# Performance work log

Measured on AMD Instinct MI355X. Metric: run time of the kernel, lower is better.

Reference implementation:

```python
import jax, jax.numpy as jnp
import numpy as np
from jax import lax

EPS = 1e-6


def layernorm2d(x, w, b):
    # channel LayerNorm over dim C of NCHW (biased variance), matching LayerNormFunction
    mu = jnp.mean(x, axis=1, keepdims=True)
    var = jnp.mean((x - mu) ** 2, axis=1, keepdims=True)
    y = (x - mu) * lax.rsqrt(var + EPS)
    return w[None, :, None, None] * y + b[None, :, None, None]


def conv1x1(x, W, b):
    # x: (N,C,H,W), W: (O,C), b: (O,)
    return jnp.einsum('nchw,oc->nohw', x, W) + b[None, :, None, None]


def conv3x3(x, W, b):
    # W: (O,I,3,3)
    y = lax.conv_general_dilated(x, W, window_strides=(1, 1), padding='SAME',
                                 dimension_numbers=('NCHW', 'OIHW', 'NCHW'))
    return y + b[None, :, None, None]


def avg_pool3x3(x):
    # torch F.avg_pool2d k=3, s=1, p=1, count_include_pad=True -> always divide by 9
    s = lax.reduce_window(x, 0.0, lax.add, (1, 1, 3, 3), (1, 1, 1, 1),
                          [(0, 0), (0, 0), (1, 1), (1, 1)])
    return s / 9.0


def setup_inputs() -> dict:
    key = jax.random.key(0)
    N, C, H, W = 8, 64, 128, 256
    ks = jax.random.split(key, 12)
    d = {
        'x_l': jax.random.normal(ks[0], (N, C, H, W), jnp.float32),
        'x_r': jax.random.normal(ks[1], (N, C, H, W), jnp.float32),
        'nl_w': jnp.ones((C,), jnp.float32),
        'nl_b': jnp.zeros((C,), jnp.float32),
        'nr_w': jnp.ones((C,), jnp.float32),
        'nr_b': jnp.zeros((C,), jnp.float32),
        'Wq_l': jax.random.normal(ks[2], (C, C), jnp.float32) * 0.05,
        'bq_l': jax.random.normal(ks[3], (C,), jnp.float32) * 0.05,
        'Wq_r': jax.random.normal(ks[4], (C, C), jnp.float32) * 0.05,
        'bq_r': jax.random.normal(ks[5], (C,), jnp.float32) * 0.05,
        'Wv_r': jax.random.normal(ks[6], (C, C), jnp.float32) * 0.05,
        'bv_r': jax.random.normal(ks[7], (C,), jnp.float32) * 0.05,
        'beta': jax.random.normal(ks[8], (1, C, 1, 1), jnp.float32) * 0.1,
        'gamma': jax.random.normal(ks[9], (1, C, 1, 1), jnp.float32) * 0.1,
        'W_hf': jax.random.normal(ks[10], (C, C, 3, 3), jnp.float32) * 0.02,
        'b_hf': jax.random.normal(ks[11], (C,), jnp.float32) * 0.02,
    }
    return d


def reference(x_l, x_r, nl_w, nl_b, nr_w, nr_b, Wq_l, bq_l, Wq_r, bq_r,
              Wv_r, bv_r, beta, gamma, W_hf, b_hf):
    C = x_l.shape[1]
    scale = C ** (-0.5)

    # Projections (1x1 convs); Q_l, Q_r, V_r as (N,H,W,C)
    Q_l = jnp.transpose(conv1x1(layernorm2d(x_l, nl_w, nl_b), Wq_l, bq_l), (0, 2, 3, 1))
    Q_r = jnp.transpose(conv1x1(layernorm2d(x_r, nr_w, nr_b), Wq_r, bq_r), (0, 2, 3, 1))
    V_r = jnp.transpose(conv1x1(x_r, Wv_r, bv_r), (0, 2, 3, 1))

    # Per-scanline cross attention: (N,H,W,W)
    attn = jnp.einsum('nhwc,nhvc->nhwv', Q_l, Q_r) * scale
    attn = jax.nn.softmax(attn, axis=-1)
    F_r2l = jnp.einsum('nhwv,nhvc->nhwc', attn, V_r)  # (N,H,W,C)
    F_r2l = jnp.transpose(F_r2l, (0, 3, 1, 2)) * beta  # (N,C,H,W)

    # High-frequency branch
    hf = conv3x3(x_r - avg_pool3x3(x_r), W_hf, b_hf)

    return x_l + F_r2l + gamma * hf
```

## Files before the change

### kernel.cpp

```cpp
#include <hip/hip_runtime.h>
#include <hip/hip_bf16.h>

#define N_ 8
#define C_ 64
#define H_ 128
#define W_ 256
#define HW_ (H_*W_)
#define CHW_ (C_*H_*W_)

typedef unsigned int u32;
typedef unsigned short u16;
typedef float f32x4 __attribute__((ext_vector_type(4)));
typedef short bf16x8 __attribute__((ext_vector_type(8)));

__device__ __forceinline__ float blo(u32 u) { return __uint_as_float(u << 16); }
__device__ __forceinline__ float bhi(u32 u) { return __uint_as_float(u & 0xffff0000u); }
__device__ __forceinline__ u16 f2bf(float f) {
    u32 u = __float_as_uint(f);
    u32 lsb = (u >> 16) & 1u;
    u += 0x7fffu + lsb;
    return (u16)(u >> 16);
}
__device__ __forceinline__ u32 pack2(float a, float b) {
    return (u32)f2bf(a) | ((u32)f2bf(b) << 16);
}
__device__ __forceinline__ int rmap(int px) {
    return (px & 0xF8) | ((px + (px >> 3)) & 7);
}

__global__ __launch_bounds__(512) void k_fused(
    const float* __restrict__ xl, const float* __restrict__ xr,
    const float* __restrict__ nlw, const float* __restrict__ nlb,
    const float* __restrict__ nrw, const float* __restrict__ nrb,
    const float* __restrict__ Wql, const float* __restrict__ bql,
    const float* __restrict__ Wqr, const float* __restrict__ bqr,
    const float* __restrict__ Wvr, const float* __restrict__ bvr,
    const float* __restrict__ beta, float* __restrict__ out)
{
    __shared__ u32 B1[8192];
    __shared__ u32 B2[8192];
    __shared__ uint4 Ks[2048];
    __shared__ float muA[256], rsA[256];
    __shared__ float SlA[64], BlA[64], SrA[64], BrA[64], BvA[64];
    const int tid  = threadIdx.x;
    const int lane = tid & 63, wv = tid >> 6;
    const int l15  = lane & 15, kg = lane >> 4;
    const int mw   = wv & 3;
    const int nh   = wv >> 2;
    const int blk  = blockIdx.x;
    const int n = blk >> 7, h = blk & 127;
    const size_t gbase = (size_t)n*CHW_ + (size_t)h*W_;

    if (tid < 64) {
        const int o = tid;
        float sl = 0.f, bl = bql[o], sr = 0.f, br = bqr[o];
        for (int c = 0; c < 64; ++c) {
            float wl = Wql[o*64+c], wr = Wqr[o*64+c];
            sl += wl * nlw[c];
            bl += wl * nlb[c];
            sr += wr * nrw[c];
            br += wr * nrb[c];
        }
        SlA[o] = sl; BlA[o] = bl; SrA[o] = sr; BrA[o] = br; BvA[o] = bvr[o];
    }

    const int oA = mw*16 + l15;
    bf16x8 aL[2], aR[2], aV[2];
    #pragma unroll
    for (int hf = 0; hf < 2; ++hf) {
        bf16x8 tl, tr, tv;
        #pragma unroll
        for (int j = 0; j < 8; ++j) {
            const int c = hf*32 + kg*8 + j;
            tl[j] = (short)f2bf(Wql[oA*64+c] * nlw[c]);
            tr[j] = (short)f2bf(Wqr[oA*64+c] * nrw[c]);
            tv[j] = (short)f2bf(Wvr[oA*64+c]);
        }
        aL[hf] = tl; aR[hf] = tr; aV[hf] = tv;
    }

    {
        const int chunk = tid >> 6;
        const int j = tid & 63;
        const int c0 = chunk*8;
        float4 v[8];
        #pragma unroll
        for (int e = 0; e < 8; ++e)
            v[e] = *(const float4*)(xl + gbase + (size_t)(c0+e)*HW_ + j*4);
        #pragma unroll
        for (int t = 0; t < 4; ++t) {
            const int px = j*4 + t;
            const int r = rmap(px);
            u32 q0,q1,q2,q3;
            const float* f0 = (const float*)&v[0]; const float* f1 = (const float*)&v[1];
            const float* f2 = (const float*)&v[2]; const float* f3 = (const float*)&v[3];
            const float* f4 = (const float*)&v[4]; const float* f5 = (const float*)&v[5];
            const float* f6 = (const float*)&v[6]; const float* f7 = (const float*)&v[7];
            asm("v_cvt_pk_bf16_f32 %0, %1, %2" : "=v"(q0) : "v"(f0[t]), "v"(f1[t]));
            asm("v_cvt_pk_bf16_f32 %0, %1, %2" : "=v"(q1) : "v"(f2[t]), "v"(f3[t]));
            asm("v_cvt_pk_bf16_f32 %0, %1, %2" : "=v"(q2) : "v"(f4[t]), "v"(f5[t]));
            asm("v_cvt_pk_bf16_f32 %0, %1, %2" : "=v"(q3) : "v"(f6[t]), "v"(f7[t]));
            uint4 pv; pv.x=q0; pv.y=q1; pv.z=q2; pv.w=q3;
            *(uint4*)&B1[r*32 + ((chunk ^ (r&7))<<2)] = pv;
        }
    }
    __syncthreads();
    if (tid < 256) {
        const int px = tid;
        const int r = rmap(px);
        float sum = 0.f, ssq = 0.f;
        #pragma unroll
        for (int c8 = 0; c8 < 8; ++c8) {
            uint4 val = *(const uint4*)&B1[r*32 + ((c8 ^ (r&7))<<2)];
            const u32* wp = (const u32*)&val;
            #pragma unroll
            for (int q = 0; q < 4; ++q) {
                float a = blo(wp[q]), b = bhi(wp[q]);
                sum += a + b; ssq += a*a + b*b;
            }
        }
        float mu = sum * (1.f/64.f);
        float var = ssq * (1.f/64.f) - mu*mu;
        muA[px] = mu;
        rsA[px] = rsqrtf(var + 1e-6f);
    }
    __syncthreads();
    {
        float Sv[4], Bv[4];
        #pragma unroll
        for (int r4 = 0; r4 < 4; ++r4) {
            Sv[r4] = SlA[mw*16 + kg*4 + r4];
            Bv[r4] = BlA[mw*16 + kg*4 + r4];
        }
        #pragma unroll
        for (int nt2 = 0; nt2 < 8; ++nt2) {
            const int nt = nh*8 + nt2;
            const int px = nt*16 + l15;
            const int r = rmap(px);
            f32x4 d = {0.f,0.f,0.f,0.f};
            #pragma unroll
            for (int hf = 0; hf < 2; ++hf) {
                bf16x8 b = *(const bf16x8*)&B1[r*32 + (((hf*4+kg) ^ (r&7))<<2)];
                d = __builtin_amdgcn_mfma_f32_16x16x32_bf16(aL[hf], b, d, 0, 0, 0);
            }
            const float mu = muA[px], rs = rsA[px];
            uint2 pv;
            pv.x = pack2(rs*(d[0] - mu*Sv[0]) + Bv[0], rs*(d[1] - mu*Sv[1]) + Bv[1]);
            pv.y = pack2(rs*(d[2] - mu*Sv[2]) + Bv[2], rs*(d[3] - mu*Sv[3]) + Bv[3]);
            const int ci = (mw*2 + (kg>>1)) ^ (px & 7);
            *(uint2*)&B2[px*32 + (ci<<2) + (kg&1)*2] = pv;
        }
    }
    __syncthreads();

    bf16x8 qf[2][2];
    #pragma unroll
    for (int ntq = 0; ntq < 2; ++ntq)
        #pragma unroll
        for (int ci = 0; ci < 2; ++ci) {
            const int q = wv*32 + ntq*16 + l15;
            qf[ntq][ci] = *(const bf16x8*)&B2[q*32 + (((ci*4+kg) ^ (q&7))<<2)];
        }
    {
        const int chunk = tid >> 6;
        const int j = tid & 63;
        const int c0 = chunk*8;
        float4 v[8];
        #pragma unroll
        for (int e = 0; e < 8; ++e)
            v[e] = *(const float4*)(xr + gbase + (size_t)(c0+e)*HW_ + j*4);
        #pragma unroll
        for (int t = 0; t < 4; ++t) {
            const int px = j*4 + t;
            const int r = rmap(px);
            u32 q0,q1,q2,q3;
            const float* f0 = (const float*)&v[0]; const float* f1 = (const float*)&v[1];
            const float* f2 = (const float*)&v[2]; const float* f3 = (const float*)&v[3];
            const float* f4 = (const float*)&v[4]; const float* f5 = (const float*)&v[5];
            const float* f6 = (const float*)&v[6]; const float* f7 = (const float*)&v[7];
            asm("v_cvt_pk_bf16_f32 %0, %1, %2" : "=v"(q0) : "v"(f0[t]), "v"(f1[t]));
            asm("v_cvt_pk_bf16_f32 %0, %1, %2" : "=v"(q1) : "v"(f2[t]), "v"(f3[t]));
            asm("v_cvt_pk_bf16_f32 %0, %1, %2" : "=v"(q2) : "v"(f4[t]), "v"(f5[t]));
            asm("v_cvt_pk_bf16_f32 %0, %1, %2" : "=v"(q3) : "v"(f6[t]), "v"(f7[t]));
            uint4 pv; pv.x=q0; pv.y=q1; pv.z=q2; pv.w=q3;
            *(uint4*)&B1[r*32 + ((chunk ^ (r&7))<<2)] = pv;
        }
    }
    __syncthreads();
    if (tid < 256) {
        const int px = tid;
        const int r = rmap(px);
        float sum = 0.f, ssq = 0.f;
        #pragma unroll
        for (int c8 = 0; c8 < 8; ++c8) {
            uint4 val = *(const uint4*)&B1[r*32 + ((c8 ^ (r&7))<<2)];
            const u32* wp = (const u32*)&val;
            #pragma unroll
            for (int q = 0; q < 4; ++q) {
                float a = blo(wp[q]), b = bhi(wp[q]);
                sum += a + b; ssq += a*a + b*b;
            }
        }
        float mu = sum * (1.f/64.f);
        float var = ssq * (1.f/64.f) - mu*mu;
        muA[px] = mu;
        rsA[px] = rsqrtf(var + 1e-6f);
    }
    __syncthreads();
    {
        float Sv[4], Bv[4];
        #pragma unroll
        for (int r4 = 0; r4 < 4; ++r4) {
            Sv[r4] = SrA[mw*16 + kg*4 + r4];
            Bv[r4] = BrA[mw*16 + kg*4 + r4];
        }
        const int chv = mw*16 + l15;
        const float vbias = BvA[chv];
        u32* KsW = (u32*)Ks;
        u16* Vts = (u16*)B2;
        #pragma unroll
        for (int nt2 = 0; nt2 < 8; ++nt2) {
            const int nt = nh*8 + nt2;
            const int px = nt*16 + l15;
            const int r = rmap(px);
            bf16x8 bX[2];
            #pragma unroll
            for (int hf = 0; hf < 2; ++hf)
                bX[hf] = *(const bf16x8*)&B1[r*32 + (((hf*4+kg) ^ (r&7))<<2)];
            f32x4 dq = {0.f,0.f,0.f,0.f};
            f32x4 dv = {0.f,0.f,0.f,0.f};
            #pragma unroll
            for (int hf = 0; hf < 2; ++hf) {
                dq = __builtin_amdgcn_mfma_f32_16x16x32_bf16(aR[hf], bX[hf], dq, 0, 0, 0);
                dv = __builtin_amdgcn_mfma_f32_16x16x32_bf16(bX[hf], aV[hf], dv, 0, 0, 0);
            }
            const float mu = muA[px], rs = rsA[px];
            uint2 pq;
            pq.x = pack2(rs*(dq[0] - mu*Sv[0]) + Bv[0], rs*(dq[1] - mu*Sv[1]) + Bv[1]);
            pq.y = pack2(rs*(dq[2] - mu*Sv[2]) + Bv[2], rs*(dq[3] - mu*Sv[3]) + Bv[3]);
            const int ciq = (mw*2 + (kg>>1)) ^ (px & 7);
            *(uint2*)&KsW[px*32 + (ciq<<2) + (kg&1)*2] = pq;
            uint2 pw;
            pw.x = pack2(dv[0] + vbias, dv[1] + vbias);
            pw.y = pack2(dv[2] + vbias, dv[3] + vbias);
            const int swz = (nt*2 + (kg>>1)) ^ (chv & 7);
            *(uint2*)&Vts[chv*256 + (swz<<3) + (kg&1)*4] = pw;
        }
    }
    __syncthreads();

    f32x4 oacc[2][4];
    #pragma unroll
    for (int a = 0; a < 2; ++a)
        #pragma unroll
        for (int b = 0; b < 4; ++b)
            oacc[a][b] = (f32x4){0.f,0.f,0.f,0.f};
    float lsum[2] = {0.f,0.f};
    u32* Pw = &B1[wv*512];
    const u16* Vts = (const u16*)B2;

    for (int kb = 0; kb < 8; ++kb) {
        f32x4 st[2][2];
        #pragma unroll
        for (int mt = 0; mt < 2; ++mt)
            #pragma unroll
            for (int nt = 0; nt < 2; ++nt)
                st[mt][nt] = (f32x4){0.f,0.f,0.f,0.f};
        #pragma unroll
        for (int ci = 0; ci < 2; ++ci) {
            bf16x8 a0 = *(const bf16x8*)&Ks[(kb*32 +      l15)*8 + ((ci*4 + kg) ^ (l15 & 7))];
            bf16x8 a1 = *(const bf16x8*)&Ks[(kb*32 + 16 + l15)*8 + ((ci*4 + kg) ^ (l15 & 7))];
            #pragma unroll
            for (int nt = 0; nt < 2; ++nt) {
                st[0][nt] = __builtin_amdgcn_mfma_f32_16x16x32_bf16(a0, qf[nt][ci], st[0][nt], 0, 0, 0);
                st[1][nt] = __builtin_amdgcn_mfma_f32_16x16x32_bf16(a1, qf[nt][ci], st[1][nt], 0, 0, 0);
            }
        }
        #pragma unroll
        for (int nt = 0; nt < 2; ++nt) {
            const int ql = nt*16 + l15;
            #pragma unroll
            for (int mt = 0; mt < 2; ++mt) {
                float p0 = __expf(st[mt][nt][0]*0.125f);
                float p1 = __expf(st[mt][nt][1]*0.125f);
                float p2 = __expf(st[mt][nt][2]*0.125f);
                float p3 = __expf(st[mt][nt][3]*0.125f);
                lsum[nt] += (p0+p1)+(p2+p3);
                u32 pr0, pr1;
                asm("v_cvt_pk_bf16_f32 %0, %1, %2" : "=v"(pr0) : "v"(p0), "v"(p1));
                asm("v_cvt_pk_bf16_f32 %0, %1, %2" : "=v"(pr1) : "v"(p2), "v"(p3));
                const int c16 = (2*mt + (kg >> 1)) ^ (ql & 3);
                uint2 pv; pv.x = pr0; pv.y = pr1;
                *(uint2*)&Pw[ql*16 + c16*4 + (kg & 1)*2] = pv;
            }
        }
        asm volatile("s_waitcnt lgkmcnt(0)" ::: "memory");
        bf16x8 vb[4];
        #pragma unroll
        for (int nc = 0; nc < 4; ++nc)
            vb[nc] = *(const bf16x8*)&Vts[(nc*16 + l15)*256 + ((kb*4 + kg) ^ (l15 & 7))*8];
        #pragma unroll
        for (int qt = 0; qt < 2; ++qt) {
            const int ql = qt*16 + l15;
            bf16x8 pa = *(const bf16x8*)&Pw[ql*16 + (kg ^ (ql & 3))*4];
            #pragma unroll
            for (int nc = 0; nc < 4; ++nc)
                oacc[qt][nc] = __builtin_amdgcn_mfma_f32_16x16x32_bf16(pa, vb[nc], oacc[qt][nc], 0, 0, 0);
        }
    }

    #pragma unroll
    for (int nt = 0; nt < 2; ++nt) {
        float s = lsum[nt];
        s += __shfl_xor(s, 16, 64);
        s += __shfl_xor(s, 32, 64);
        lsum[nt] = s;
    }
    float linv[2][4];
    #pragma unroll
    for (int qt = 0; qt < 2; ++qt)
        #pragma unroll
        for (int r = 0; r < 4; ++r)
            linv[qt][r] = 1.0f / __shfl(lsum[qt], kg*4 + r, 64);

    float* PwF = (float*)Pw;
    const size_t obase = gbase + wv*32;
    #pragma unroll
    for (int nc = 0; nc < 4; ++nc) {
        asm volatile("s_waitcnt lgkmcnt(0)" ::: "memory");
        #pragma unroll
        for (int qt = 0; qt < 2; ++qt) {
            f32x4 vals;
            vals[0] = oacc[qt][nc][0]*linv[qt][0];
            vals[1] = oacc[qt][nc][1]*linv[qt][1];
            vals[2] = oacc[qt][nc][2]*linv[qt][2];
            vals[3] = oacc[qt][nc][3]*linv[qt][3];
            *(f32x4*)&PwF[l15*32 + (((qt*4 + kg) ^ (l15 & 7))<<2)] = vals;
        }
        asm volatile("s_waitcnt lgkmcnt(0)" ::: "memory");
        #pragma unroll
        for (int it = 0; it < 8; ++it) {
            const int csub = it*2 + (lane >> 5);
            const int qloc = lane & 31;
            float v = PwF[csub*32 + ((((qloc >> 2)) ^ (csub & 7))<<2) + (qloc & 3)];
            const int ch = nc*16 + csub;
            size_t gidx = obase + (size_t)ch*HW_ + qloc;
            out[gidx] = xl[gidx] + beta[ch]*v + out[gidx];
        }
    }
}

__global__ __launch_bounds__(256) void k_hipass(
    const float* __restrict__ xr, u16* __restrict__ Tt)
{
    __shared__ u16 Ts[64*256];
    const int bid = blockIdx.x;
    const int blk = (bid & 7)*128 + (bid >> 3);
    const int n = blk >> 7, h = blk & 127;
    const int tid = threadIdx.x;
    const int lane = tid & 63, wv = tid >> 6;
    const float* rowp = xr + (size_t)n*CHW_ + (size_t)h*W_ + lane*4;

    #pragma unroll
    for (int ci = 0; ci < 16; ++ci) {
        const int c = wv*16 + ci;
        const float* pc = rowp + (size_t)c*HW_;
        float ctr0=0.f, ctr1=0.f, ctr2=0.f, ctr3=0.f;
        float s0=0.f, s1=0.f, s2=0.f, s3=0.f;
        #pragma unroll
        for (int dy = -1; dy <= 1; ++dy) {
            const int hh = h + dy;
            float4 v = {0.f,0.f,0.f,0.f};
            if (hh >= 0 && hh < 128) v = *(const float4*)(pc + dy*W_);
            float lft = __shfl_up(v.w, 1);
            float rgt = __shfl_down(v.x, 1);
            if (lane == 0)  lft = 0.f;
            if (lane == 63) rgt = 0.f;
            s0 += lft + v.x + v.y;
            s1 += v.x + v.y + v.z;
            s2 += v.y + v.z + v.w;
            s3 += v.z + v.w + rgt;
            if (dy == 0) { ctr0=v.x; ctr1=v.y; ctr2=v.z; ctr3=v.w; }
        }
        uint2 pv;
        pv.x = pack2(ctr0 - s0*(1.f/9.f), ctr1 - s1*(1.f/9.f));
        pv.y = pack2(ctr2 - s2*(1.f/9.f), ctr3 - s3*(1.f/9.f));
        const int swz = (c >> 3) << 3;
        *(uint2*)&Ts[c*256 + ((lane*4) ^ swz)] = pv;
    }
    __syncthreads();
    uint4* gout = (uint4*)(Tt + (size_t)blk*256*64);
    #pragma unroll
    for (int iter = 0; iter < 8; ++iter) {
        const int lin = iter*256 + tid;
        const int px = lin >> 3, chunk = lin & 7;
        const int pxs = px ^ (chunk << 3);
        u32 w4[4];
        #pragma unroll
        for (int tp = 0; tp < 4; ++tp) {
            const int c0 = chunk*8 + tp*2;
            u16 a = Ts[(c0    )*256 + pxs];
            u16 b = Ts[(c0 + 1)*256 + pxs];
            w4[tp] = (u32)a | ((u32)b << 16);
        }
        uint4 v; v.x=w4[0]; v.y=w4[1]; v.z=w4[2]; v.w=w4[3];
        gout[lin] = v;
    }
}

__device__ __forceinline__ void conv_tile(
    const uint4* __restrict__ buf, const bf16x8* A,
    const float* gv, const float* bv,
    int n, int h, int w0, int mt, int l15, int kg,
    float* __restrict__ out)
{
    f32x4 acc[4] = {{0,0,0,0},{0,0,0,0},{0,0,0,0},{0,0,0,0}};
    #pragma unroll
    for (int s = 0; s < 18; ++s) {
        const int q  = s >> 1;
        const int dy = q / 3, dx = q % 3;
        const int c0 = (s & 1)*4 + kg;
        #pragma unroll
        for (int nt = 0; nt < 4; ++nt) {
            const int wt = nt*16 + l15 + dx;
            bf16x8 b = *(const bf16x8*)&buf[(dy*66 + wt)*8 + (c0 ^ (wt & 7))];
            acc[nt] = __builtin_amdgcn_mfma_f32_16x16x32_bf16(A[s], b, acc[nt], 0, 0, 0);
        }
    }
    #pragma unroll
    for (int nt = 0; nt < 4; ++nt) {
        const int px = w0 + nt*16 + l15;
        #pragma unroll
        for (int r = 0; r < 4; ++r) {
            const int oo = mt*16 + kg*4 + r;
            size_t idx = (size_t)(n*64 + oo)*HW_ + (size_t)h*W_ + px;
            out[idx] = gv[r]*(acc[nt][r] + bv[r]);
        }
    }
}

__global__ __launch_bounds__(256) void k_conv(
    const u16* __restrict__ Tt, const float* __restrict__ Whf,
    const float* __restrict__ bhf, const float* __restrict__ gam,
    float* __restrict__ out)
{
    __shared__ uint4 Xs[2][1584];
    const int tid  = threadIdx.x;
    const int lane = tid & 63;
    const int mt   = tid >> 6;
    const int l15  = lane & 15;
    const int kg   = lane >> 4;
    const int bid  = blockIdx.x;
    const int blk2 = (bid & 7)*256 + (bid >> 3);
    const int row  = blk2 >> 1, half = blk2 & 1;
    const int n = row >> 7, h = row & 127;
    const int w00 = half*128;
    const int w01 = w00 + 64;

    const int oa = mt*16 + l15;
    bf16x8 A[18];
    #pragma unroll
    for (int s = 0; s < 18; ++s) {
        const int q  = s >> 1;
        const int ib = (s & 1)*32 + kg*8;
        bf16x8 a;
        #pragma unroll
        for (int j = 0; j < 8; ++j) {
            float wv = Whf[(size_t)(oa*64 + ib + j)*9 + q];
            a[j] = (short)f2bf(wv);
        }
        A[s] = a;
    }
    float gv[4], bv[4];
    #pragma unroll
    for (int r = 0; r < 4; ++r) {
        int oo = mt*16 + kg*4 + r;
        gv[r] = gam[oo];
        bv[r] = bhf[oo];
    }

    for (int it = tid; it < 1584; it += 256) {
        int dy    = it / 528;
        int rem   = it - dy*528;
        int wt    = rem >> 3;
        int chunk = rem & 7;
        int hh = h + dy - 1;
        int wg = w00 + wt - 1;
        uint4 v = {0,0,0,0};
        if (hh >= 0 && hh < 128 && wg >= 0 && wg < 256)
            v = *(const uint4*)(Tt + (((size_t)(n*128 + hh)*256 + wg)*64 + chunk*8));
        Xs[0][(dy*66 + wt)*8 + (chunk ^ (wt & 7))] = v;
    }
    __syncthreads();

    uint4 rr[7];
    #pragma unroll
    for (int k = 0; k < 7; ++k) {
        const int it = k*256 + tid;
        if (it < 1584) {
            int dy    = it / 528;
            int rem   = it - dy*528;
            int wt    = rem >> 3;
            int chunk = rem & 7;
            int hh = h + dy - 1;
            int wg = w01 + wt - 1;
            uint4 v = {0,0,0,0};
            if (hh >= 0 && hh < 128 && wg >= 0 && wg < 256)
                v = *(const uint4*)(Tt + (((size_t)(n*128 + hh)*256 + wg)*64 + chunk*8));
            rr[k] = v;
        }
    }

    conv_tile(&Xs[0][0], A, gv, bv, n, h, w00, mt, l15, kg, out);

    #pragma unroll
    for (int k = 0; k < 7; ++k) {
        const int it = k*256 + tid;
        if (it < 1584) {
            int dy    = it / 528;
            int rem   = it - dy*528;
            int wt    = rem >> 3;
            int chunk = rem & 7;
            Xs[1][(dy*66 + wt)*8 + (chunk ^ (wt & 7))] = rr[k];
        }
    }
    __syncthreads();
    conv_tile(&Xs[1][0], A, gv, bv, n, h, w01, mt, l15, kg, out);
}

extern "C" void kernel_launch(void* const* d_in, const int* in_sizes, int n_in,
                              void* d_out, int out_size, void* d_ws, size_t ws_size,
                              hipStream_t stream)
{
    const float* xl   = (const float*)d_in[0];
    const float* xr   = (const float*)d_in[1];
    const float* nlw  = (const float*)d_in[2];
    const float* nlb  = (const float*)d_in[3];
    const float* nrw  = (const float*)d_in[4];
    const float* nrb  = (const float*)d_in[5];
    const float* Wql  = (const float*)d_in[6];
    const float* bql  = (const float*)d_in[7];
    const float* Wqr  = (const float*)d_in[8];
    const float* bqr  = (const float*)d_in[9];
    const float* Wvr  = (const float*)d_in[10];
    const float* bvr  = (const float*)d_in[11];
    const float* beta = (const float*)d_in[12];
    const float* gam  = (const float*)d_in[13];
    const float* Whf  = (const float*)d_in[14];
    const float* bhf  = (const float*)d_in[15];
    float* out = (float*)d_out;

    u16* Tt = (u16*)d_ws;

    k_hipass<<<1024, 256, 0, stream>>>(xr, Tt);
    k_conv<<<2048, 256, 0, stream>>>(Tt, Whf, bhf, gam, out);
    k_fused<<<1024, 512, 0, stream>>>(xl, xr, nlw, nlb, nrw, nrb,
                                      Wql, bql, Wqr, bqr, Wvr, bvr,
                                      beta, out);
}
```

Before: 176.5 us.

## Split block into left/right wave halves processing both projections concurrently

The block's 8 waves are split into two halves: waves 0-3 load x_l, compute its layernorm stats and the Q_l projection, while waves 4-7 do the same for x_r plus K and V. Previously these ran one after another with all waves. This removes several barriers and serial phases, so the global loads for both images overlap. In exchange, each wave now holds 16 tiles of packed Q/V results in registers before writing them to shared memory, which raises register pressure.

Measured after the change: 200.4 us. 1.14x slower.

```diff
diff --git a/kernel.cpp b/kernel.cpp
--- a/kernel.cpp
+++ b/kernel.cpp
@@ -39,14 +39,15 @@
 {
     __shared__ u32 B1[8192];
     __shared__ u32 B2[8192];
-    __shared__ uint4 Ks[2048];
-    __shared__ float muA[256], rsA[256];
+    __shared__ u32 B3[8192];
+    __shared__ float muL[256], rsL[256], muR[256], rsR[256];
     __shared__ float SlA[64], BlA[64], SrA[64], BrA[64], BvA[64];
     const int tid  = threadIdx.x;
     const int lane = tid & 63, wv = tid >> 6;
     const int l15  = lane & 15, kg = lane >> 4;
+    const int side = wv >> 2;
     const int mw   = wv & 3;
-    const int nh   = wv >> 2;
+    const int htid = tid & 255;
     const int blk  = blockIdx.x;
     const int n = blk >> 7, h = blk & 127;
     const size_t gbase = (size_t)n*CHW_ + (size_t)h*W_;
@@ -66,52 +67,73 @@
 
     const int oA = mw*16 + l15;
     bf16x8 aL[2], aR[2], aV[2];
-    #pragma unroll
-    for (int hf = 0; hf < 2; ++hf) {
-        bf16x8 tl, tr, tv;
-        #pragma unroll
-        for (int j = 0; j < 8; ++j) {
-            const int c = hf*32 + kg*8 + j;
-            tl[j] = (short)f2bf(Wql[oA*64+c] * nlw[c]);
-            tr[j] = (short)f2bf(Wqr[oA*64+c] * nrw[c]);
-            tv[j] = (short)f2bf(Wvr[oA*64+c]);
-        }
-        aL[hf] = tl; aR[hf] = tr; aV[hf] = tv;
+    if (side == 0) {
+        #pragma unroll
+        for (int hf = 0; hf < 2; ++hf) {
+            bf16x8 tl;
+            #pragma unroll
+            for (int j = 0; j < 8; ++j) {
+                const int c = hf*32 + kg*8 + j;
+                tl[j] = (short)f2bf(Wql[oA*64+c] * nlw[c]);
+            }
+            aL[hf] = tl;
+        }
+    } else {
+        #pragma unroll
+        for (int hf = 0; hf < 2; ++hf) {
+            bf16x8 tr, tv;
+            #pragma unroll
+            for (int j = 0; j < 8; ++j) {
+                const int c = hf*32 + kg*8 + j;
+                tr[j] = (short)f2bf(Wqr[oA*64+c] * nrw[c]);
+                tv[j] = (short)f2bf(Wvr[oA*64+c]);
+            }
+            aR[hf] = tr; aV[hf] = tv;
+        }
     }
 
     {
-        const int chunk = tid >> 6;
-        const int j = tid & 63;
-        const int c0 = chunk*8;
-        float4 v[8];
-        #pragma unroll
-        for (int e = 0; e < 8; ++e)
-            v[e] = *(const float4*)(xl + gbase + (size_t)(c0+e)*HW_ + j*4);
-        #pragma unroll
-        for (int t = 0; t < 4; ++t) {
-            const int px = j*4 + t;
-            const int r = rmap(px);
-            u32 q0,q1,q2,q3;
-            const float* f0 = (const float*)&v[0]; const float* f1 = (const float*)&v[1];
-            const float* f2 = (const float*)&v[2]; const float* f3 = (const float*)&v[3];
-            const float* f4 = (const float*)&v[4]; const float* f5 = (const float*)&v[5];
-            const float* f6 = (const float*)&v[6]; const float* f7 = (const float*)&v[7];
-            asm("v_cvt_pk_bf16_f32 %0, %1, %2" : "=v"(q0) : "v"(f0[t]), "v"(f1[t]));
-            asm("v_cvt_pk_bf16_f32 %0, %1, %2" : "=v"(q1) : "v"(f2[t]), "v"(f3[t]));
-            asm("v_cvt_pk_bf16_f32 %0, %1, %2" : "=v"(q2) : "v"(f4[t]), "v"(f5[t]));
-            asm("v_cvt_pk_bf16_f32 %0, %1, %2" : "=v"(q3) : "v"(f6[t]), "v"(f7[t]));
-            uint4 pv; pv.x=q0; pv.y=q1; pv.z=q2; pv.w=q3;
-            *(uint4*)&B1[r*32 + ((chunk ^ (r&7))<<2)] = pv;
-        }
-    }
-    __syncthreads();
-    if (tid < 256) {
-        const int px = tid;
+        const float* xsrc = side ? xr : xl;
+        u32* XB = side ? B2 : B1;
+        #pragma unroll
+        for (int it2 = 0; it2 < 2; ++it2) {
+            const int g = it2*256 + htid;
+            const int chunk = g >> 6;
+            const int j = g & 63;
+            const int c0 = chunk*8;
+            float4 v[8];
+            #pragma unroll
+            for (int e = 0; e < 8; ++e)
+                v[e] = *(const float4*)(xsrc + gbase + (size_t)(c0+e)*HW_ + j*4);
+            #pragma unroll
+            for (int t = 0; t < 4; ++t) {
+                const int px = j*4 + t;
+                const int r = rmap(px);
+                u32 q0,q1,q2,q3;
+                const float* f0 = (const float*)&v[0]; const float* f1 = (const float*)&v[1];
+                const float* f2 = (const float*)&v[2]; const float* f3 = (const float*)&v[3];
+                const float* f4 = (const float*)&v[4]; const float* f5 = (const float*)&v[5];
+                const float* f6 = (const float*)&v[6]; const float* f7 = (const float*)&v[7];
+                asm("v_cvt_pk_bf16_f32 %0, %1, %2" : "=v"(q0) : "v"(f0[t]), "v"(f1[t]));
+                asm("v_cvt_pk_bf16_f32 %0, %1, %2" : "=v"(q1) : "v"(f2[t]), "v"(f3[t]));
+                asm("v_cvt_pk_bf16_f32 %0, %1, %2" : "=v"(q2) : "v"(f4[t]), "v"(f5[t]));
+                asm("v_cvt_pk_bf16_f32 %0, %1, %2" : "=v"(q3) : "v"(f6[t]), "v"(f7[t]));
+                uint4 pv; pv.x=q0; pv.y=q1; pv.z=q2; pv.w=q3;
+                *(uint4*)&XB[r*32 + ((chunk ^ (r&7))<<2)] = pv;
+            }
+        }
+    }
+    __syncthreads();
+    {
+        const u32* XB = side ? B2 : B1;
+        float* muX = side ? muR : muL;
+        float* rsX = side ? rsR : rsL;
+        const int px = htid;
         const int r = rmap(px);
         float sum = 0.f, ssq = 0.f;
         #pragma unroll
         for (int c8 = 0; c8 < 8; ++c8) {
-            uint4 val = *(const uint4*)&B1[r*32 + ((c8 ^ (r&7))<<2)];
+            uint4 val = *(const uint4*)&XB[r*32 + ((c8 ^ (r&7))<<2)];
             const u32* wp = (const u32*)&val;
             #pragma unroll
             for (int q = 0; q < 4; ++q) {
@@ -121,11 +143,13 @@
         }
         float mu = sum * (1.f/64.f);
         float var = ssq * (1.f/64.f) - mu*mu;
-        muA[px] = mu;
-        rsA[px] = rsqrtf(var + 1e-6f);
-    }
-    __syncthreads();
-    {
+        muX[px] = mu;
+        rsX[px] = rsqrtf(var + 1e-6f);
+    }
+    __syncthreads();
+
+    u32 hq[16][2], hv[16][2];
+    if (side == 0) {
         float Sv[4], Bv[4];
         #pragma unroll
         for (int r4 = 0; r4 < 4; ++r4) {
@@ -133,8 +157,7 @@
             Bv[r4] = BlA[mw*16 + kg*4 + r4];
         }
         #pragma unroll
-        for (int nt2 = 0; nt2 < 8; ++nt2) {
-            const int nt = nh*8 + nt2;
+        for (int nt = 0; nt < 16; ++nt) {
             const int px = nt*16 + l15;
             const int r = rmap(px);
             f32x4 d = {0.f,0.f,0.f,0.f};
@@ -143,71 +166,14 @@
                 bf16x8 b = *(const bf16x8*)&B1[r*32 + (((hf*4+kg) ^ (r&7))<<2)];
                 d = __builtin_amdgcn_mfma_f32_16x16x32_bf16(aL[hf], b, d, 0, 0, 0);
             }
-            const float mu = muA[px], rs = rsA[px];
+            const float mu = muL[px], rs = rsL[px];
             uint2 pv;
             pv.x = pack2(rs*(d[0] - mu*Sv[0]) + Bv[0], rs*(d[1] - mu*Sv[1]) + Bv[1]);
             pv.y = pack2(rs*(d[2] - mu*Sv[2]) + Bv[2], rs*(d[3] - mu*Sv[3]) + Bv[3]);
             const int ci = (mw*2 + (kg>>1)) ^ (px & 7);
-            *(uint2*)&B2[px*32 + (ci<<2) + (kg&1)*2] = pv;
-        }
-    }
-    __syncthreads();
-
-    bf16x8 qf[2][2];
-    #pragma unroll
-    for (int ntq = 0; ntq < 2; ++ntq)
-        #pragma unroll
-        for (int ci = 0; ci < 2; ++ci) {
-            const int q = wv*32 + ntq*16 + l15;
-            qf[ntq][ci] = *(const bf16x8*)&B2[q*32 + (((ci*4+kg) ^ (q&7))<<2)];
-        }
-    {
-        const int chunk = tid >> 6;
-        const int j = tid & 63;
-        const int c0 = chunk*8;
-        float4 v[8];
-        #pragma unroll
-        for (int e = 0; e < 8; ++e)
-            v[e] = *(const float4*)(xr + gbase + (size_t)(c0+e)*HW_ + j*4);
-        #pragma unroll
-        for (int t = 0; t < 4; ++t) {
-            const int px = j*4 + t;
-            const int r = rmap(px);
-            u32 q0,q1,q2,q3;
-            const float* f0 = (const float*)&v[0]; const float* f1 = (const float*)&v[1];
-            const float* f2 = (const float*)&v[2]; const float* f3 = (const float*)&v[3];
-            const float* f4 = (const float*)&v[4]; const float* f5 = (const float*)&v[5];
-            const float* f6 = (const float*)&v[6]; const float* f7 = (const float*)&v[7];
-            asm("v_cvt_pk_bf16_f32 %0, %1, %2" : "=v"(q0) : "v"(f0[t]), "v"(f1[t]));
-            asm("v_cvt_pk_bf16_f32 %0, %1, %2" : "=v"(q1) : "v"(f2[t]), "v"(f3[t]));
-            asm("v_cvt_pk_bf16_f32 %0, %1, %2" : "=v"(q2) : "v"(f4[t]), "v"(f5[t]));
-            asm("v_cvt_pk_bf16_f32 %0, %1, %2" : "=v"(q3) : "v"(f6[t]), "v"(f7[t]));
-            uint4 pv; pv.x=q0; pv.y=q1; pv.z=q2; pv.w=q3;
-            *(uint4*)&B1[r*32 + ((chunk ^ (r&7))<<2)] = pv;
-        }
-    }
-    __syncthreads();
-    if (tid < 256) {
-        const int px = tid;
-        const int r = rmap(px);
-        float sum = 0.f, ssq = 0.f;
-        #pragma unroll
-        for (int c8 = 0; c8 < 8; ++c8) {
-            uint4 val = *(const uint4*)&B1[r*32 + ((c8 ^ (r&7))<<2)];
-            const u32* wp = (const u32*)&val;
-            #pragma unroll
-            for (int q = 0; q < 4; ++q) {
-                float a = blo(wp[q]), b = bhi(wp[q]);
-                sum += a + b; ssq += a*a + b*b;
-            }
-        }
-        float mu = sum * (1.f/64.f);
-        float var = ssq * (1.f/64.f) - mu*mu;
-        muA[px] = mu;
-        rsA[px] = rsqrtf(var + 1e-6f);
-    }
-    __syncthreads();
-    {
+            *(uint2*)&B3[px*32 + (ci<<2) + (kg&1)*2] = pv;
+        }
+    } else {
         float Sv[4], Bv[4];
         #pragma unroll
         for (int r4 = 0; r4 < 4; ++r4) {
@@ -216,17 +182,14 @@
         }
         const int chv = mw*16 + l15;
         const float vbias = BvA[chv];
-        u32* KsW = (u32*)Ks;
-        u16* Vts = (u16*)B2;
-        #pragma unroll
-        for (int nt2 = 0; nt2 < 8; ++nt2) {
-            const int nt = nh*8 + nt2;
+        #pragma unroll
+        for (int nt = 0; nt < 16; ++nt) {
             const int px = nt*16 + l15;
             const int r = rmap(px);
             bf16x8 bX[2];
             #pragma unroll
             for (int hf = 0; hf < 2; ++hf)
-                bX[hf] = *(const bf16x8*)&B1[r*32 + (((hf*4+kg) ^ (r&7))<<2)];
+                bX[hf] = *(const bf16x8*)&B2[r*32 + (((hf*4+kg) ^ (r&7))<<2)];
             f32x4 dq = {0.f,0.f,0.f,0.f};
             f32x4 dv = {0.f,0.f,0.f,0.f};
             #pragma unroll
@@ -234,19 +197,38 @@
                 dq = __builtin_amdgcn_mfma_f32_16x16x32_bf16(aR[hf], bX[hf], dq, 0, 0, 0);
                 dv = __builtin_amdgcn_mfma_f32_16x16x32_bf16(bX[hf], aV[hf], dv, 0, 0, 0);
             }
-            const float mu = muA[px], rs = rsA[px];
-            uint2 pq;
-            pq.x = pack2(rs*(dq[0] - mu*Sv[0]) + Bv[0], rs*(dq[1] - mu*Sv[1]) + Bv[1]);
-            pq.y = pack2(rs*(dq[2] - mu*Sv[2]) + Bv[2], rs*(dq[3] - mu*Sv[3]) + Bv[3]);
+            const float mu = muR[px], rs = rsR[px];
+            hq[nt][0] = pack2(rs*(dq[0] - mu*Sv[0]) + Bv[0], rs*(dq[1] - mu*Sv[1]) + Bv[1]);
+            hq[nt][1] = pack2(rs*(dq[2] - mu*Sv[2]) + Bv[2], rs*(dq[3] - mu*Sv[3]) + Bv[3]);
+            hv[nt][0] = pack2(dv[0] + vbias, dv[1] + vbias);
+            hv[nt][1] = pack2(dv[2] + vbias, dv[3] + vbias);
+        }
+    }
+    __syncthreads();
+
+    if (side == 1) {
+        u32* KsW = B2;
+        u16* Vts16 = (u16*)B1;
+        const int chv = mw*16 + l15;
+        #pragma unroll
+        for (int nt = 0; nt < 16; ++nt) {
+            const int px = nt*16 + l15;
             const int ciq = (mw*2 + (kg>>1)) ^ (px & 7);
+            uint2 pq; pq.x = hq[nt][0]; pq.y = hq[nt][1];
             *(uint2*)&KsW[px*32 + (ciq<<2) + (kg&1)*2] = pq;
-            uint2 pw;
-            pw.x = pack2(dv[0] + vbias, dv[1] + vbias);
-            pw.y = pack2(dv[2] + vbias, dv[3] + vbias);
+            uint2 pw; pw.x = hv[nt][0]; pw.y = hv[nt][1];
             const int swz = (nt*2 + (kg>>1)) ^ (chv & 7);
-            *(uint2*)&Vts[chv*256 + (swz<<3) + (kg&1)*4] = pw;
-        }
-    }
+            *(uint2*)&Vts16[chv*256 + (swz<<3) + (kg&1)*4] = pw;
+        }
+    }
+    bf16x8 qf[2][2];
+    #pragma unroll
+    for (int ntq = 0; ntq < 2; ++ntq)
+        #pragma unroll
+        for (int ci = 0; ci < 2; ++ci) {
+            const int q = wv*32 + ntq*16 + l15;
+            qf[ntq][ci] = *(const bf16x8*)&B3[q*32 + (((ci*4+kg) ^ (q&7))<<2)];
+        }
     __syncthreads();
 
     f32x4 oacc[2][4];
@@ -256,8 +238,9 @@
         for (int b = 0; b < 4; ++b)
             oacc[a][b] = (f32x4){0.f,0.f,0.f,0.f};
     float lsum[2] = {0.f,0.f};
-    u32* Pw = &B1[wv*512];
-    const u16* Vts = (const u16*)B2;
+    u32* Pw = &B3[wv*512];
+    const u16* Vts = (const u16*)B1;
+    const uint4* KsR = (const uint4*)B2;
 
     for (int kb = 0; kb < 8; ++kb) {
         f32x4 st[2][2];
@@ -268,8 +251,8 @@
                 st[mt][nt] = (f32x4){0.f,0.f,0.f,0.f};
         #pragma unroll
         for (int ci = 0; ci < 2; ++ci) {
-            bf16x8 a0 = *(const bf16x8*)&Ks[(kb*32 +      l15)*8 + ((ci*4 + kg) ^ (l15 & 7))];
-            bf16x8 a1 = *(const bf16x8*)&Ks[(kb*32 + 16 + l15)*8 + ((ci*4 + kg) ^ (l15 & 7))];
+            bf16x8 a0 = *(const bf16x8*)&KsR[(kb*32 +      l15)*8 + ((ci*4 + kg) ^ (l15 & 7))];
+            bf16x8 a1 = *(const bf16x8*)&KsR[(kb*32 + 16 + l15)*8 + ((ci*4 + kg) ^ (l15 & 7))];
             #pragma unroll
             for (int nt = 0; nt < 2; ++nt) {
                 st[0][nt] = __builtin_amdgcn_mfma_f32_16x16x32_bf16(a0, qf[nt][ci], st[0][nt], 0, 0, 0);
```

## Drop K LDS buffer, pass P via shuffles, store output directly from registers

Applied to the files above, without the earlier changes.

Removes the separate 32KB Ks shared buffer by holding the projected Q/V values in registers, then writing K into B1 after a barrier. This cuts LDS per block, and the launch bound is raised to request 4 blocks per SM. The softmax probability tile is now redistributed into the MFMA A-operand layout with cross-lane shuffles instead of an LDS round trip. The epilogue writes float4 vectors straight from the accumulators, skipping the LDS transpose. The trade-off is higher register pressure under the tighter launch bound, plus an extra barrier.

After: 191.9 us. +8.7%, slower.

```diff
diff --git a/kernel.cpp b/kernel.cpp
--- a/kernel.cpp
+++ b/kernel.cpp
@@ -28,7 +28,7 @@
     return (px & 0xF8) | ((px + (px >> 3)) & 7);
 }
 
-__global__ __launch_bounds__(512) void k_fused(
+__global__ __launch_bounds__(512, 4) void k_fused(
     const float* __restrict__ xl, const float* __restrict__ xr,
     const float* __restrict__ nlw, const float* __restrict__ nlb,
     const float* __restrict__ nrw, const float* __restrict__ nrb,
@@ -39,7 +39,6 @@
 {
     __shared__ u32 B1[8192];
     __shared__ u32 B2[8192];
-    __shared__ uint4 Ks[2048];
     __shared__ float muA[256], rsA[256];
     __shared__ float SlA[64], BlA[64], SrA[64], BrA[64], BvA[64];
     const int tid  = threadIdx.x;
@@ -207,6 +206,8 @@
         rsA[px] = rsqrtf(var + 1e-6f);
     }
     __syncthreads();
+
+    u32 hq[8][2], hv[8][2];
     {
         float Sv[4], Bv[4];
         #pragma unroll
@@ -216,8 +217,6 @@
         }
         const int chv = mw*16 + l15;
         const float vbias = BvA[chv];
-        u32* KsW = (u32*)Ks;
-        u16* Vts = (u16*)B2;
         #pragma unroll
         for (int nt2 = 0; nt2 < 8; ++nt2) {
             const int nt = nh*8 + nt2;
@@ -235,16 +234,26 @@
                 dv = __builtin_amdgcn_mfma_f32_16x16x32_bf16(bX[hf], aV[hf], dv, 0, 0, 0);
             }
             const float mu = muA[px], rs = rsA[px];
-            uint2 pq;
-            pq.x = pack2(rs*(dq[0] - mu*Sv[0]) + Bv[0], rs*(dq[1] - mu*Sv[1]) + Bv[1]);
-            pq.y = pack2(rs*(dq[2] - mu*Sv[2]) + Bv[2], rs*(dq[3] - mu*Sv[3]) + Bv[3]);
+            hq[nt2][0] = pack2(rs*(dq[0] - mu*Sv[0]) + Bv[0], rs*(dq[1] - mu*Sv[1]) + Bv[1]);
+            hq[nt2][1] = pack2(rs*(dq[2] - mu*Sv[2]) + Bv[2], rs*(dq[3] - mu*Sv[3]) + Bv[3]);
+            hv[nt2][0] = pack2(dv[0] + vbias, dv[1] + vbias);
+            hv[nt2][1] = pack2(dv[2] + vbias, dv[3] + vbias);
+        }
+    }
+    __syncthreads();
+    {
+        const int chv = mw*16 + l15;
+        u16* Vts16 = (u16*)B2;
+        #pragma unroll
+        for (int nt2 = 0; nt2 < 8; ++nt2) {
+            const int nt = nh*8 + nt2;
+            const int px = nt*16 + l15;
             const int ciq = (mw*2 + (kg>>1)) ^ (px & 7);
-            *(uint2*)&KsW[px*32 + (ciq<<2) + (kg&1)*2] = pq;
-            uint2 pw;
-            pw.x = pack2(dv[0] + vbias, dv[1] + vbias);
-            pw.y = pack2(dv[2] + vbias, dv[3] + vbias);
+            uint2 pq; pq.x = hq[nt2][0]; pq.y = hq[nt2][1];
+            *(uint2*)&B1[px*32 + (ciq<<2) + (kg&1)*2] = pq;
+            uint2 pw; pw.x = hv[nt2][0]; pw.y = hv[nt2][1];
             const int swz = (nt*2 + (kg>>1)) ^ (chv & 7);
-            *(uint2*)&Vts[chv*256 + (swz<<3) + (kg&1)*4] = pw;
+            *(uint2*)&Vts16[chv*256 + (swz<<3) + (kg&1)*4] = pw;
         }
     }
     __syncthreads();
@@ -256,8 +265,9 @@
         for (int b = 0; b < 4; ++b)
             oacc[a][b] = (f32x4){0.f,0.f,0.f,0.f};
     float lsum[2] = {0.f,0.f};
-    u32* Pw = &B1[wv*512];
+    const uint4* KsR = (const uint4*)B1;
     const u16* Vts = (const u16*)B2;
+    const int srcA = ((2*kg) & 3)*16 + l15;
 
     for (int kb = 0; kb < 8; ++kb) {
         f32x4 st[2][2];
@@ -268,45 +278,56 @@
                 st[mt][nt] = (f32x4){0.f,0.f,0.f,0.f};
         #pragma unroll
         for (int ci = 0; ci < 2; ++ci) {
-            bf16x8 a0 = *(const bf16x8*)&Ks[(kb*32 +      l15)*8 + ((ci*4 + kg) ^ (l15 & 7))];
-            bf16x8 a1 = *(const bf16x8*)&Ks[(kb*32 + 16 + l15)*8 + ((ci*4 + kg) ^ (l15 & 7))];
+            bf16x8 a0 = *(const bf16x8*)&KsR[(kb*32 +      l15)*8 + ((ci*4 + kg) ^ (l15 & 7))];
+            bf16x8 a1 = *(const bf16x8*)&KsR[(kb*32 + 16 + l15)*8 + ((ci*4 + kg) ^ (l15 & 7))];
             #pragma unroll
             for (int nt = 0; nt < 2; ++nt) {
                 st[0][nt] = __builtin_amdgcn_mfma_f32_16x16x32_bf16(a0, qf[nt][ci], st[0][nt], 0, 0, 0);
                 st[1][nt] = __builtin_amdgcn_mfma_f32_16x16x32_bf16(a1, qf[nt][ci], st[1][nt], 0, 0, 0);
             }
         }
+        bf16x8 paR[2];
         #pragma unroll
         for (int nt = 0; nt < 2; ++nt) {
-            const int ql = nt*16 + l15;
-            #pragma unroll
-            for (int mt = 0; mt < 2; ++mt) {
-                float p0 = __expf(st[mt][nt][0]*0.125f);
-                float p1 = __expf(st[mt][nt][1]*0.125f);
-                float p2 = __expf(st[mt][nt][2]*0.125f);
-                float p3 = __expf(st[mt][nt][3]*0.125f);
-                lsum[nt] += (p0+p1)+(p2+p3);
-                u32 pr0, pr1;
-                asm("v_cvt_pk_bf16_f32 %0, %1, %2" : "=v"(pr0) : "v"(p0), "v"(p1));
-                asm("v_cvt_pk_bf16_f32 %0, %1, %2" : "=v"(pr1) : "v"(p2), "v"(p3));
-                const int c16 = (2*mt + (kg >> 1)) ^ (ql & 3);
-                uint2 pv; pv.x = pr0; pv.y = pr1;
-                *(uint2*)&Pw[ql*16 + c16*4 + (kg & 1)*2] = pv;
-            }
-        }
-        asm volatile("s_waitcnt lgkmcnt(0)" ::: "memory");
+            float p00 = __expf(st[0][nt][0]*0.125f);
+            float p01 = __expf(st[0][nt][1]*0.125f);
+            float p02 = __expf(st[0][nt][2]*0.125f);
+            float p03 = __expf(st[0][nt][3]*0.125f);
+            float p10 = __expf(st[1][nt][0]*0.125f);
+            float p11 = __expf(st[1][nt][1]*0.125f);
+            float p12 = __expf(st[1][nt][2]*0.125f);
+            float p13 = __expf(st[1][nt][3]*0.125f);
+            lsum[nt] += ((p00+p01)+(p02+p03)) + ((p10+p11)+(p12+p13));
+            u32 pk00, pk01, pk10, pk11;
+            asm("v_cvt_pk_bf16_f32 %0, %1, %2" : "=v"(pk00) : "v"(p00), "v"(p01));
+            asm("v_cvt_pk_bf16_f32 %0, %1, %2" : "=v"(pk01) : "v"(p02), "v"(p03));
+            asm("v_cvt_pk_bf16_f32 %0, %1, %2" : "=v"(pk10) : "v"(p10), "v"(p11));
+            asm("v_cvt_pk_bf16_f32 %0, %1, %2" : "=v"(pk11) : "v"(p12), "v"(p13));
+            int a00 = __shfl((int)pk00, srcA, 64);
+            int a01 = __shfl((int)pk01, srcA, 64);
+            int a10 = __shfl((int)pk10, srcA, 64);
+            int a11 = __shfl((int)pk11, srcA, 64);
+            int b00 = __shfl((int)pk00, srcA + 16, 64);
+            int b01 = __shfl((int)pk01, srcA + 16, 64);
+            int b10 = __shfl((int)pk10, srcA + 16, 64);
+            int b11 = __shfl((int)pk11, srcA + 16, 64);
+            const bool lo = (kg < 2);
+            union { u32 u[4]; bf16x8 v; } pu;
+            pu.u[0] = (u32)(lo ? a00 : a10);
+            pu.u[1] = (u32)(lo ? a01 : a11);
+            pu.u[2] = (u32)(lo ? b00 : b10);
+            pu.u[3] = (u32)(lo ? b01 : b11);
+            paR[nt] = pu.v;
+        }
         bf16x8 vb[4];
         #pragma unroll
         for (int nc = 0; nc < 4; ++nc)
             vb[nc] = *(const bf16x8*)&Vts[(nc*16 + l15)*256 + ((kb*4 + kg) ^ (l15 & 7))*8];
         #pragma unroll
-        for (int qt = 0; qt < 2; ++qt) {
-            const int ql = qt*16 + l15;
-            bf16x8 pa = *(const bf16x8*)&Pw[ql*16 + (kg ^ (ql & 3))*4];
+        for (int qt = 0; qt < 2; ++qt)
             #pragma unroll
             for (int nc = 0; nc < 4; ++nc)
-                oacc[qt][nc] = __builtin_amdgcn_mfma_f32_16x16x32_bf16(pa, vb[nc], oacc[qt][nc], 0, 0, 0);
-        }
+                oacc[qt][nc] = __builtin_amdgcn_mfma_f32_16x16x32_bf16(paR[qt], vb[nc], oacc[qt][nc], 0, 0, 0);
     }
 
     #pragma unroll
@@ -323,29 +344,21 @@
         for (int r = 0; r < 4; ++r)
             linv[qt][r] = 1.0f / __shfl(lsum[qt], kg*4 + r, 64);
 
-    float* PwF = (float*)Pw;
-    const size_t obase = gbase + wv*32;
+    const size_t qbase = gbase + wv*32;
     #pragma unroll
     for (int nc = 0; nc < 4; ++nc) {
-        asm volatile("s_waitcnt lgkmcnt(0)" ::: "memory");
+        const int ch = nc*16 + l15;
+        const float bch = beta[ch];
         #pragma unroll
         for (int qt = 0; qt < 2; ++qt) {
+            const size_t gidx = qbase + (size_t)ch*HW_ + qt*16 + kg*4;
+            f32x4 o4 = *(const f32x4*)&out[gidx];
+            f32x4 x4 = *(const f32x4*)&xl[gidx];
             f32x4 vals;
-            vals[0] = oacc[qt][nc][0]*linv[qt][0];
-            vals[1] = oacc[qt][nc][1]*linv[qt][1];
-            vals[2] = oacc[qt][nc][2]*linv[qt][2];
-            vals[3] = oacc[qt][nc][3]*linv[qt][3];
-            *(f32x4*)&PwF[l15*32 + (((qt*4 + kg) ^ (l15 & 7))<<2)] = vals;
-        }
-        asm volatile("s_waitcnt lgkmcnt(0)" ::: "memory");
-        #pragma unroll
-        for (int it = 0; it < 8; ++it) {
-            const int csub = it*2 + (lane >> 5);
-            const int qloc = lane & 31;
-            float v = PwF[csub*32 + ((((qloc >> 2)) ^ (csub & 7))<<2) + (qloc & 3)];
-            const int ch = nc*16 + csub;
-            size_t gidx = obase + (size_t)ch*HW_ + qloc;
-            out[gidx] = xl[gidx] + beta[ch]*v + out[gidx];
+            #pragma unroll
+            for (int r = 0; r < 4; ++r)
+                vals[r] = x4[r] + bch*(oacc[qt][nc][r]*linv[qt][r]) + o4[r];
+            *(f32x4*)&out[gidx] = vals;
         }
     }
 }
```
